# Performance work log

Hardware: AMD Instinct MI355X
Metric: run time of the kernel (lower is better)

The kernel has to match this reference:

```python
import jax, jax.numpy as jnp
import numpy as np

N_NODES = 100_000
D_FEAT = 64
N_RAND_EDGES = 1_600_000  # plus N_NODES self-loops (dgl.add_self_loop)


def setup_inputs() -> dict:
    key = jax.random.key(0)
    k1, k2, k3 = jax.random.split(key, 3)
    features = jax.random.normal(k1, (N_NODES, D_FEAT), dtype=jnp.float32)
    src = jax.random.randint(k2, (N_RAND_EDGES,), 0, N_NODES, dtype=jnp.int32)
    dst = jax.random.randint(k3, (N_RAND_EDGES,), 0, N_NODES, dtype=jnp.int32)
    loops = jnp.arange(N_NODES, dtype=jnp.int32)
    src = jnp.concatenate([src, loops])  # [1.7M]
    dst = jnp.concatenate([dst, loops])
    return {"features": features, "src": src, "dst": dst}


def reference(features, src, dst):
    # LightConv with norm='both': x * deg_out^-0.5 -> copy_src+sum -> * deg_in^-0.5
    n = features.shape[0]
    ones = jnp.ones(src.shape[0], dtype=features.dtype)
    deg_out = jnp.clip(jax.ops.segment_sum(ones, src, num_segments=n), 1.0)
    deg_in = jnp.clip(jax.ops.segment_sum(ones, dst, num_segments=n), 1.0)
    x = features * (deg_out ** -0.5)[:, None]          # pre-normalize by src out-degree
    agg = jax.ops.segment_sum(x[src], dst, num_segments=n)  # SpMM: gather src rows, scatter-add to dst
    return agg * (deg_in ** -0.5)[:, None]             # post-normalize by dst in-degree
```

## Files before the change

### kernel.cpp

```cpp
#include <hip/hip_runtime.h>
#include <hip/hip_bf16.h>

#define N_NODES 100000
#define D_FEAT 64
#define CAP 64
#define NBD 784
#define DB_CAP 3072
#define NBS 392
#define SB_CAP 5500
#define PT 512
#define EPT 7

typedef unsigned int uint;
typedef unsigned short ushort;

__device__ __forceinline__ uint f2bf(float f) {
    uint u = __float_as_uint(f);
    return (u + 0x7fffu + ((u >> 16) & 1u)) >> 16;
}

__global__ __launch_bounds__(PT) void
partition_kernel(const int* __restrict__ src, const int* __restrict__ dst,
                 int* __restrict__ dstCur, int* __restrict__ srcCur,
                 uint* __restrict__ dstrec, ushort* __restrict__ srcrec,
                 int nE) {
    __shared__ int hd[NBD], bd[NBD], hs[NBS], bs[NBS];
    const int t = threadIdx.x;
    for (int i = t; i < NBD; i += PT) hd[i] = 0;
    for (int i = t; i < NBS; i += PT) hs[i] = 0;
    __syncthreads();
    const int beg = blockIdx.x * (EPT * PT);
    int se[EPT], de[EPT], rd[EPT], rs[EPT];
#pragma unroll
    for (int k = 0; k < EPT; ++k) {
        int e = beg + t + k * PT;
        int s = 0, d = 0, r1 = 0, r2 = 0;
        if (e < nE) {
            s = src[e]; d = dst[e];
            r1 = atomicAdd(&hd[d >> 7], 1);
            r2 = atomicAdd(&hs[s >> 8], 1);
        }
        se[k] = s; de[k] = d; rd[k] = r1; rs[k] = r2;
    }
    __syncthreads();
    for (int i = t; i < NBD; i += PT) bd[i] = atomicAdd(&dstCur[i], hd[i]);
    for (int i = t; i < NBS; i += PT) bs[i] = atomicAdd(&srcCur[i], hs[i]);
    __syncthreads();
#pragma unroll
    for (int k = 0; k < EPT; ++k) {
        int e = beg + t + k * PT;
        if (e < nE) {
            int d = de[k], s = se[k];
            int p = bd[d >> 7] + rd[k];
            if (p < DB_CAP)
                dstrec[(size_t)(d >> 7) * DB_CAP + p] = ((uint)(d & 127) << 17) | (uint)s;
            int p2 = bs[s >> 8] + rs[k];
            if (p2 < SB_CAP)
                srcrec[(size_t)(s >> 8) * SB_CAP + p2] = (ushort)(s & 255);
        }
    }
}

__global__ __launch_bounds__(512) void
prescale_kernel(const ushort* __restrict__ srcrec, const int* __restrict__ srcCur,
                const float* __restrict__ feat, uint2* __restrict__ xb, int n) {
    __shared__ int lc[256];
    const int t = threadIdx.x;
    const int b = blockIdx.x;
    const int base = b << 8;
    if (t < 256) lc[t] = 0;
    __syncthreads();
    int cnt = min(srcCur[b], SB_CAP);
    const uint* rec2 = (const uint*)(srcrec + (size_t)b * SB_CAP);
    const int pairs = cnt >> 1;
    for (int i = t; i < pairs; i += 512) {
        uint rr = rec2[i];
        atomicAdd(&lc[rr & 0xFFu], 1);
        atomicAdd(&lc[(rr >> 16) & 0xFFu], 1);
    }
    if ((cnt & 1) && t == 0)
        atomicAdd(&lc[srcrec[(size_t)b * SB_CAP + cnt - 1]], 1);
    __syncthreads();
    const int rows = min(256, n + 1 - base);
    const int d4 = t & 15;
    for (int r = t >> 4; r < rows; r += 32) {
        const int row = base + r;
        uint2 o;
        if (row == n) {
            o.x = 0u; o.y = 0u;
        } else {
            float w = rsqrtf((float)max(lc[r], 1));
            float4 v = ((const float4*)feat)[(size_t)row * 16 + d4];
            o.x = f2bf(w * v.x) | (f2bf(w * v.y) << 16);
            o.y = f2bf(w * v.z) | (f2bf(w * v.w) << 16);
        }
        xb[(size_t)row * 16 + d4] = o;
    }
}

__global__ __launch_bounds__(512) void
binGather_kernel(const uint* __restrict__ dstrec, const int* __restrict__ dstCur,
                 const uint2* __restrict__ xb, float* __restrict__ out, int n) {
    __shared__ int cnt[128], off[128];
    __shared__ int eLDS[DB_CAP];
    const int t = threadIdx.x;
    const int b = blockIdx.x;
    const int base = b << 7;
    if (t < 128) cnt[t] = 0;
    __syncthreads();
    const int nr = min(dstCur[b], DB_CAP);
    const uint* rec = dstrec + (size_t)b * DB_CAP;
    for (int i = t; i < nr; i += 512) atomicAdd(&cnt[rec[i] >> 17], 1);
    __syncthreads();
    if (t < 64) {
        int v0 = cnt[t], v1 = cnt[64 + t];
        int s0 = v0, s1 = v1;
        for (int d = 1; d < 64; d <<= 1) {
            int u0 = __shfl_up(s0, d, 64);
            int u1 = __shfl_up(s1, d, 64);
            if (t >= d) { s0 += u0; s1 += u1; }
        }
        int tot0 = __shfl(s0, 63, 64);
        off[t]      = s0 - v0;
        off[64 + t] = tot0 + s1 - v1;
    }
    __syncthreads();
    for (int i = t; i < nr; i += 512) {
        uint r = rec[i];
        int p = atomicAdd(&off[r >> 17], 1);
        eLDS[p] = (int)(r & 0x1FFFF);
    }
    __syncthreads();
    const int wv = t >> 6, lane = t & 63, sub = lane >> 4, d4 = lane & 15;
    for (int k = 0; k < 16; ++k) {
        const int r = wv + (k << 3);
        const int row = base + r;
        if (row >= n) continue;
        const int c = cnt[r];
        const int start = off[r] - c;
        float4 acc = {0.f, 0.f, 0.f, 0.f};
        int i = sub;
        for (; i + 4 < c; i += 8) {
            int s0 = eLDS[start + i];
            int s1 = eLDS[start + i + 4];
            uint2 v0 = xb[(size_t)s0 * 16 + d4];
            uint2 v1 = xb[(size_t)s1 * 16 + d4];
            acc.x += __uint_as_float(v0.x << 16);
            acc.y += __uint_as_float(v0.x & 0xffff0000u);
            acc.z += __uint_as_float(v0.y << 16);
            acc.w += __uint_as_float(v0.y & 0xffff0000u);
            acc.x += __uint_as_float(v1.x << 16);
            acc.y += __uint_as_float(v1.x & 0xffff0000u);
            acc.z += __uint_as_float(v1.y << 16);
            acc.w += __uint_as_float(v1.y & 0xffff0000u);
        }
        if (i < c) {
            int s0 = eLDS[start + i];
            uint2 v0 = xb[(size_t)s0 * 16 + d4];
            acc.x += __uint_as_float(v0.x << 16);
            acc.y += __uint_as_float(v0.x & 0xffff0000u);
            acc.z += __uint_as_float(v0.y << 16);
            acc.w += __uint_as_float(v0.y & 0xffff0000u);
        }
        for (int o = 16; o < 64; o <<= 1) {
            acc.x += __shfl_xor(acc.x, o, 64);
            acc.y += __shfl_xor(acc.y, o, 64);
            acc.z += __shfl_xor(acc.z, o, 64);
            acc.w += __shfl_xor(acc.w, o, 64);
        }
        if (sub == 0) {
            float si = rsqrtf((float)max(c, 1));
            float4 rr = { acc.x * si, acc.y * si, acc.z * si, acc.w * si };
            ((float4*)out)[(size_t)row * 16 + d4] = rr;
        }
    }
}

__global__ void bucket_kernel(const int* __restrict__ src, const int* __restrict__ dst,
                              int* __restrict__ cursor, int* __restrict__ deg_out,
                              int* __restrict__ edge_src, int nE) {
    int e = blockIdx.x * blockDim.x + threadIdx.x;
    if (e < nE) {
        int s = src[e];
        int d = dst[e];
        atomicAdd(&deg_out[s], 1);
        int pos = atomicAdd(&cursor[d], 1);
        if (pos < CAP) edge_src[(size_t)d * CAP + pos] = s;
    }
}

__global__ void gather_cap_kernel(const float* __restrict__ feat,
                                  const int* __restrict__ edge_src,
                                  const int* __restrict__ cursor,
                                  const int* __restrict__ deg_out,
                                  float* __restrict__ out, int n) {
    int wave = (blockIdx.x * blockDim.x + threadIdx.x) >> 6;
    if (wave >= n) return;
    int lane = threadIdx.x & 63;
    int cnt = min(cursor[wave], CAP);

    int   s_l = (lane < cnt) ? edge_src[(size_t)wave * CAP + lane] : 0;
    float w_l = (lane < cnt) ? rsqrtf((float)max(deg_out[s_l], 1)) : 0.0f;

    int sub = lane >> 4;
    int d4  = lane & 15;
    float4 a0 = {0.f,0.f,0.f,0.f}, a1 = {0.f,0.f,0.f,0.f};

    for (int i = 0; i < cnt; i += 8) {
        int   s0 = __shfl(s_l, i + sub, 64);
        float w0 = __shfl(w_l, i + sub, 64);
        int   s1 = __shfl(s_l, i + sub + 4, 64);
        float w1 = __shfl(w_l, i + sub + 4, 64);
        float4 v0 = ((const float4*)feat)[(size_t)s0 * 16 + d4];
        float4 v1 = ((const float4*)feat)[(size_t)s1 * 16 + d4];
        a0.x += w0 * v0.x; a0.y += w0 * v0.y; a0.z += w0 * v0.z; a0.w += w0 * v0.w;
        a1.x += w1 * v1.x; a1.y += w1 * v1.y; a1.z += w1 * v1.z; a1.w += w1 * v1.w;
    }
    float4 acc = { a0.x + a1.x, a0.y + a1.y, a0.z + a1.z, a0.w + a1.w };
    for (int off = 16; off < 64; off <<= 1) {
        acc.x += __shfl_xor(acc.x, off, 64);
        acc.y += __shfl_xor(acc.y, off, 64);
        acc.z += __shfl_xor(acc.z, off, 64);
        acc.w += __shfl_xor(acc.w, off, 64);
    }
    if (sub == 0) {
        float si = rsqrtf((float)max(cnt, 1));
        float4 r = { acc.x * si, acc.y * si, acc.z * si, acc.w * si };
        ((float4*)out)[(size_t)wave * 16 + d4] = r;
    }
}


extern "C" void kernel_launch(void* const* d_in, const int* in_sizes, int n_in,
                              void* d_out, int out_size, void* d_ws, size_t ws_size,
                              hipStream_t stream) {
    const float* feat = (const float*)d_in[0];
    const int*   src  = (const int*)d_in[1];
    const int*   dst  = (const int*)d_in[2];
    float* out = (float*)d_out;
    const int nE = in_sizes[1];
    const int n  = N_NODES;

    const size_t ctr_bytes = (NBD + NBS) * sizeof(int);
    const size_t dr_off    = (ctr_bytes + 511) & ~(size_t)511;
    const size_t dr_sz     = (size_t)NBD * DB_CAP * sizeof(uint);
    const size_t sr_off    = dr_off + dr_sz;
    const size_t sr_sz     = (size_t)NBS * SB_CAP * sizeof(ushort);
    const size_t xb_off    = (sr_off + sr_sz + 511) & ~(size_t)511;
    const size_t xb_bytes  = (size_t)(n + 1) * 16 * sizeof(uint2);
    const size_t need_new  = xb_off + xb_bytes;
    const size_t need_fp   = (size_t)n * (2 + CAP) * sizeof(int);

    if (ws_size >= need_new) {
        char*   W        = (char*)d_ws;
        int*    dstCur   = (int*)W;
        int*    srcCur   = dstCur + NBD;
        uint*   dstrec   = (uint*)(W + dr_off);
        ushort* srcrec   = (ushort*)(W + sr_off);
        uint2*  xb       = (uint2*)(W + xb_off);

        hipMemsetAsync(dstCur, 0, ctr_bytes, stream);
        {
            const int chunk = EPT * PT;
            const int grid = (nE + chunk - 1) / chunk;
            partition_kernel<<<grid, PT, 0, stream>>>(src, dst, dstCur, srcCur,
                                                      dstrec, srcrec, nE);
        }
        prescale_kernel<<<NBS, 512, 0, stream>>>(srcrec, srcCur, feat, xb, n);
        binGather_kernel<<<NBD, 512, 0, stream>>>(dstrec, dstCur, xb, out, n);
    } else if (ws_size >= need_fp) {
        int* cursor   = (int*)d_ws;
        int* deg_out  = cursor + n;
        int* edge_src = deg_out + n;

        hipMemsetAsync(cursor, 0, 2 * (size_t)n * sizeof(int), stream);
        {
            int block = 256, grid = (nE + block - 1) / block;
            bucket_kernel<<<grid, block, 0, stream>>>(src, dst, cursor, deg_out, edge_src, nE);
        }
        {
            int block = 256, grid = (n + 3) / 4;
            gather_cap_kernel<<<grid, block, 0, stream>>>(feat, edge_src, cursor, deg_out, out, n);
        }
    }
}
```

Baseline: 162.2 us.

## Stage partition writes through LDS for coalescing and widen gather loads to 16 bytes

The partition kernel now runs a local exclusive scan over the per-block bucket histograms and places each edge's destination record into a bucket-sorted LDS staging buffer. It then writes the records to global memory in bucket order, so stores that land in the same bucket are contiguous instead of scattered. The same is done for source records in a second pass that reuses the buffer. The gather kernel loads 16 bytes per lane (8 lanes per 64-feature bf16 row) instead of 8 bytes, processing eight edges per wave per step, with two accumulators and a wider shuffle reduction. The cost is extra LDS (about 28KB), more barriers, and scan work in the partition kernel.

```diff
diff --git a/kernel.cpp b/kernel.cpp
--- a/kernel.cpp
+++ b/kernel.cpp
@@ -25,11 +25,14 @@
                  uint* __restrict__ dstrec, ushort* __restrict__ srcrec,
                  int nE) {
     __shared__ int hd[NBD], bd[NBD], hs[NBS], bs[NBS];
+    __shared__ uint2 pairD[EPT * PT];
     const int t = threadIdx.x;
+    const int wv = t >> 6, lane = t & 63;
     for (int i = t; i < NBD; i += PT) hd[i] = 0;
     for (int i = t; i < NBS; i += PT) hs[i] = 0;
     __syncthreads();
     const int beg = blockIdx.x * (EPT * PT);
+    const int tot = min(nE - beg, EPT * PT);
     int se[EPT], de[EPT], rd[EPT], rs[EPT];
 #pragma unroll
     for (int k = 0; k < EPT; ++k) {
@@ -46,18 +49,69 @@
     for (int i = t; i < NBD; i += PT) bd[i] = atomicAdd(&dstCur[i], hd[i]);
     for (int i = t; i < NBS; i += PT) bs[i] = atomicAdd(&srcCur[i], hs[i]);
     __syncthreads();
+    if (wv == 0) {
+        int carry = 0;
+        for (int c0 = 0; c0 < NBD; c0 += 64) {
+            int idx = c0 + lane;
+            int v = (idx < NBD) ? hd[idx] : 0;
+            int sc = v;
+            for (int d = 1; d < 64; d <<= 1) {
+                int u = __shfl_up(sc, d, 64);
+                if (lane >= d) sc += u;
+            }
+            if (idx < NBD) hd[idx] = sc - v + carry;
+            carry += __shfl(sc, 63, 64);
+        }
+    } else if (wv == 1) {
+        int carry = 0;
+        for (int c0 = 0; c0 < NBS; c0 += 64) {
+            int idx = c0 + lane;
+            int v = (idx < NBS) ? hs[idx] : 0;
+            int sc = v;
+            for (int d = 1; d < 64; d <<= 1) {
+                int u = __shfl_up(sc, d, 64);
+                if (lane >= d) sc += u;
+            }
+            if (idx < NBS) hs[idx] = sc - v + carry;
+            carry += __shfl(sc, 63, 64);
+        }
+    }
+    __syncthreads();
 #pragma unroll
     for (int k = 0; k < EPT; ++k) {
         int e = beg + t + k * PT;
         if (e < nE) {
             int d = de[k], s = se[k];
-            int p = bd[d >> 7] + rd[k];
-            if (p < DB_CAP)
-                dstrec[(size_t)(d >> 7) * DB_CAP + p] = ((uint)(d & 127) << 17) | (uint)s;
-            int p2 = bs[s >> 8] + rs[k];
-            if (p2 < SB_CAP)
-                srcrec[(size_t)(s >> 8) * SB_CAP + p2] = (ushort)(s & 255);
-        }
+            int b = d >> 7;
+            int p = bd[b] + rd[k];
+            uint addr = (p < DB_CAP) ? (uint)(b * DB_CAP + p) : 0xFFFFFFFFu;
+            uint2 pr; pr.x = addr; pr.y = ((uint)(d & 127) << 17) | (uint)s;
+            pairD[hd[b] + rd[k]] = pr;
+        }
+    }
+    __syncthreads();
+    for (int j = t; j < tot; j += PT) {
+        uint2 pr = pairD[j];
+        if (pr.x != 0xFFFFFFFFu) dstrec[pr.x] = pr.y;
+    }
+    __syncthreads();
+    uint* bufS = (uint*)pairD;
+#pragma unroll
+    for (int k = 0; k < EPT; ++k) {
+        int e = beg + t + k * PT;
+        if (e < nE) {
+            int s = se[k];
+            int b2 = s >> 8;
+            int p2 = bs[b2] + rs[k];
+            uint addr = (p2 < SB_CAP) ? (uint)(b2 * SB_CAP + p2) : 0xFFFFFFu;
+            bufS[hs[b2] + rs[k]] = (addr << 8) | (uint)(s & 255);
+        }
+    }
+    __syncthreads();
+    for (int j = t; j < tot; j += PT) {
+        uint v = bufS[j];
+        uint a = v >> 8;
+        if (a < (uint)(NBS * SB_CAP)) srcrec[a] = (ushort)(v & 255);
     }
 }
 
@@ -131,47 +185,67 @@
         eLDS[p] = (int)(r & 0x1FFFF);
     }
     __syncthreads();
-    const int wv = t >> 6, lane = t & 63, sub = lane >> 4, d4 = lane & 15;
+    const int wv = t >> 6, lane = t & 63, sub8 = lane >> 3, d8 = lane & 7;
+    const uint4* xb4 = (const uint4*)xb;
     for (int k = 0; k < 16; ++k) {
         const int r = wv + (k << 3);
         const int row = base + r;
         if (row >= n) continue;
         const int c = cnt[r];
         const int start = off[r] - c;
-        float4 acc = {0.f, 0.f, 0.f, 0.f};
-        int i = sub;
-        for (; i + 4 < c; i += 8) {
+        float4 a0 = {0.f, 0.f, 0.f, 0.f};
+        float4 a1 = {0.f, 0.f, 0.f, 0.f};
+        int i = sub8;
+        for (; i + 8 < c; i += 16) {
             int s0 = eLDS[start + i];
-            int s1 = eLDS[start + i + 4];
-            uint2 v0 = xb[(size_t)s0 * 16 + d4];
-            uint2 v1 = xb[(size_t)s1 * 16 + d4];
-            acc.x += __uint_as_float(v0.x << 16);
-            acc.y += __uint_as_float(v0.x & 0xffff0000u);
-            acc.z += __uint_as_float(v0.y << 16);
-            acc.w += __uint_as_float(v0.y & 0xffff0000u);
-            acc.x += __uint_as_float(v1.x << 16);
-            acc.y += __uint_as_float(v1.x & 0xffff0000u);
-            acc.z += __uint_as_float(v1.y << 16);
-            acc.w += __uint_as_float(v1.y & 0xffff0000u);
+            int s1 = eLDS[start + i + 8];
+            uint4 v0 = xb4[(size_t)s0 * 8 + d8];
+            uint4 v1 = xb4[(size_t)s1 * 8 + d8];
+            a0.x += __uint_as_float(v0.x << 16);
+            a0.y += __uint_as_float(v0.x & 0xffff0000u);
+            a0.z += __uint_as_float(v0.y << 16);
+            a0.w += __uint_as_float(v0.y & 0xffff0000u);
+            a1.x += __uint_as_float(v0.z << 16);
+            a1.y += __uint_as_float(v0.z & 0xffff0000u);
+            a1.z += __uint_as_float(v0.w << 16);
+            a1.w += __uint_as_float(v0.w & 0xffff0000u);
+            a0.x += __uint_as_float(v1.x << 16);
+            a0.y += __uint_as_float(v1.x & 0xffff0000u);
+            a0.z += __uint_as_float(v1.y << 16);
+            a0.w += __uint_as_float(v1.y & 0xffff0000u);
+            a1.x += __uint_as_float(v1.z << 16);
+            a1.y += __uint_as_float(v1.z & 0xffff0000u);
+            a1.z += __uint_as_float(v1.w << 16);
+            a1.w += __uint_as_float(v1.w & 0xffff0000u);
         }
         if (i < c) {
             int s0 = eLDS[start + i];
-            uint2 v0 = xb[(size_t)s0 * 16 + d4];
-            acc.x += __uint_as_float(v0.x << 16);
-            acc.y += __uint_as_float(v0.x & 0xffff0000u);
-            acc.z += __uint_as_float(v0.y << 16);
-            acc.w += __uint_as_float(v0.y & 0xffff0000u);
-        }
-        for (int o = 16; o < 64; o <<= 1) {
-            acc.x += __shfl_xor(acc.x, o, 64);
-            acc.y += __shfl_xor(acc.y, o, 64);
-            acc.z += __shfl_xor(acc.z, o, 64);
-            acc.w += __shfl_xor(acc.w, o, 64);
-        }
-        if (sub == 0) {
+            uint4 v0 = xb4[(size_t)s0 * 8 + d8];
+            a0.x += __uint_as_float(v0.x << 16);
+            a0.y += __uint_as_float(v0.x & 0xffff0000u);
+            a0.z += __uint_as_float(v0.y << 16);
+            a0.w += __uint_as_float(v0.y & 0xffff0000u);
+            a1.x += __uint_as_float(v0.z << 16);
+            a1.y += __uint_as_float(v0.z & 0xffff0000u);
+            a1.z += __uint_as_float(v0.w << 16);
+            a1.w += __uint_as_float(v0.w & 0xffff0000u);
+        }
+        for (int o = 8; o < 64; o <<= 1) {
+            a0.x += __shfl_xor(a0.x, o, 64);
+            a0.y += __shfl_xor(a0.y, o, 64);
+            a0.z += __shfl_xor(a0.z, o, 64);
+            a0.w += __shfl_xor(a0.w, o, 64);
+            a1.x += __shfl_xor(a1.x, o, 64);
+            a1.y += __shfl_xor(a1.y, o, 64);
+            a1.z += __shfl_xor(a1.z, o, 64);
+            a1.w += __shfl_xor(a1.w, o, 64);
+        }
+        if (sub8 == 0) {
             float si = rsqrtf((float)max(c, 1));
-            float4 rr = { acc.x * si, acc.y * si, acc.z * si, acc.w * si };
-            ((float4*)out)[(size_t)row * 16 + d4] = rr;
+            float4 r0 = { a0.x * si, a0.y * si, a0.z * si, a0.w * si };
+            float4 r1 = { a1.x * si, a1.y * si, a1.z * si, a1.w * si };
+            ((float4*)out)[(size_t)row * 16 + d8 * 2]     = r0;
+            ((float4*)out)[(size_t)row * 16 + d8 * 2 + 1] = r1;
         }
     }
 }
```

Result: no change. 162.5 us (+0.2%).
